# Kernel optimization log

Hardware: AMD Instinct MI355X
Metric: run time of the kernel (lower is better)

Reference implementation:

```python
import jax, jax.numpy as jnp
import numpy as np

B, T, C, H = 8, 2048, 1024, 64  # batch, seq_len(block_size), embedding_size, head_size


def setup_inputs() -> dict:
    key = jax.random.key(0)
    kx, kk, kq, kv = jax.random.split(key, 4)
    x = jax.random.normal(kx, (B, T, C), dtype=jnp.float32)
    # nn.Linear(C, H, bias=False) weights, stored as [in, out] for x @ W
    s = 1.0 / np.sqrt(C)
    Wk = jax.random.uniform(kk, (C, H), dtype=jnp.float32, minval=-s, maxval=s)
    Wq = jax.random.uniform(kq, (C, H), dtype=jnp.float32, minval=-s, maxval=s)
    Wv = jax.random.uniform(kv, (C, H), dtype=jnp.float32, minval=-s, maxval=s)
    return {"x": x, "Wk": Wk, "Wq": Wq, "Wv": Wv}


def reference(x, Wk, Wq, Wv):
    Bx, Tx, Cx = x.shape
    k = jnp.einsum('btc,ch->bth', x, Wk)
    q = jnp.einsum('btc,ch->bth', x, Wq)
    v = jnp.einsum('btc,ch->bth', x, Wv)
    # NOTE: original scales by embedding dim C ** -0.5, not head_size
    scores = jnp.einsum('bth,bsh->bts', q, k) * (Cx ** -0.5)  # [B,T,T]
    causal = jnp.tril(jnp.ones((Tx, Tx), dtype=bool))
    scores = jnp.where(causal, scores, -jnp.inf)
    attn = jax.nn.softmax(scores, axis=-1)
    # dropout is identity in eval/deterministic mode
    out = jnp.einsum('bts,bsh->bth', attn, v)  # [B,T,H]
    return out
```

## Files before the change

kernel.cpp:

```cpp
#include <hip/hip_runtime.h>
#include <hip/hip_bf16.h>
#include <math.h>


#define BT 16384
#define TSEQ 2048
#define XST 72

typedef __attribute__((ext_vector_type(8))) __bf16 bf16x8;
typedef __attribute__((ext_vector_type(8))) unsigned short ushort8;
typedef __attribute__((ext_vector_type(4))) float floatx4;

#define MFMA16(a, b, c) __builtin_amdgcn_mfma_f32_16x16x32_bf16( \
    __builtin_bit_cast(bf16x8, (a)), __builtin_bit_cast(bf16x8, (b)), (c), 0, 0, 0)

__device__ inline unsigned short f2bf(float f) {
  unsigned u = __builtin_bit_cast(unsigned, f);
  u += 0x7FFFu + ((u >> 16) & 1u);
  return (unsigned short)(u >> 16);
}
__device__ inline float bf2f(unsigned short s) {
  return __builtin_bit_cast(float, (unsigned)s << 16);
}
__device__ inline unsigned long long pack4bf(floatx4 f) {
  return (unsigned long long)f2bf(f[0]) | ((unsigned long long)f2bf(f[1]) << 16) |
         ((unsigned long long)f2bf(f[2]) << 32) | ((unsigned long long)f2bf(f[3]) << 48);
}

__global__ __launch_bounds__(256) void wt2_kernel(
    const float* __restrict__ Wq, const float* __restrict__ Wk,
    const float* __restrict__ Wv, unsigned short* __restrict__ Wt2) {
  __shared__ float ls[64][65];
  const int m = blockIdx.x >> 4;
  const int kci = blockIdx.x & 15;
  const int c0 = kci << 6;
  const float* __restrict__ W = (m == 0) ? Wq : (m == 1) ? Wk : Wv;
  const int tid = threadIdx.x;
#pragma unroll
  for (int i = 0; i < 16; ++i) {
    int idx = tid + (i << 8);
    int cl = idx >> 6, h = idx & 63;
    ls[cl][h] = W[(c0 + cl) * 64 + h];
  }
  __syncthreads();
  const int w = tid >> 6, lane = tid & 63;
  const int quad = lane >> 4, l16 = lane & 15;
  const int nt = (m << 2) + w;
#pragma unroll
  for (int half = 0; half < 2; ++half) {
    ushort8 t;
#pragma unroll
    for (int j = 0; j < 8; ++j)
      t[j] = f2bf(ls[(half << 5) + (quad << 3) + j][(w << 4) + l16]);
    *(ushort8*)(Wt2 + ((size_t)(((nt << 4) + kci) * 2 + half) << 9) +
                (lane << 3)) = t;
  }
}

__global__ __launch_bounds__(256) void qkv_mfma(
    const float* __restrict__ x, const unsigned short* __restrict__ Wt2,
    unsigned short* __restrict__ Qf, unsigned short* __restrict__ Kf,
    unsigned short* __restrict__ Vf) {
  __shared__ unsigned short region[4][16 * XST];
  __shared__ float red[2][12][64][4];

  const int tid = threadIdx.x;
  const int w = tid >> 6, lane = tid & 63;
  const int quad = lane >> 4, l16 = lane & 15;
  const int r0 = blockIdx.x << 4;
  const float* __restrict__ xw = x + (size_t)r0 * 1024 + (w << 8);
  const int srow = lane >> 4, scol = (lane & 15) << 2;

  floatx4 acc[12];
#pragma unroll
  for (int i = 0; i < 12; ++i) acc[i] = (floatx4){0.f, 0.f, 0.f, 0.f};

  floatx4 pf[2][4];
#pragma unroll
  for (int i = 0; i < 4; ++i)
    pf[0][i] = *(const floatx4*)(xw + (size_t)((i << 2) + srow) * 1024 + scol);
#pragma unroll
  for (int i = 0; i < 4; ++i)
    pf[1][i] = *(const floatx4*)(xw + (size_t)((i << 2) + srow) * 1024 + 64 + scol);

  unsigned short* buf = &region[w][0];
#pragma unroll
  for (int it = 0; it < 4; ++it) {
#pragma unroll
    for (int i = 0; i < 4; ++i)
      *(unsigned long long*)&buf[((i << 2) + srow) * XST + scol] =
          pack4bf(pf[it & 1][i]);
    if (it < 2) {
#pragma unroll
      for (int i = 0; i < 4; ++i)
        pf[it & 1][i] = *(const floatx4*)(xw + (size_t)((i << 2) + srow) * 1024 +
                                          ((it + 2) << 6) + scol);
    }
    ushort8 a0 = *(const ushort8*)&buf[l16 * XST + (quad << 3)];
    ushort8 a1 = *(const ushort8*)&buf[l16 * XST + 32 + (quad << 3)];
    const int kci = (w << 2) + it;
    const unsigned short* bbase = Wt2 + ((size_t)kci << 10) + ((size_t)lane << 3);
#pragma unroll
    for (int nt = 0; nt < 12; ++nt) {
      const unsigned short* bp = bbase + ((size_t)nt << 14);
      ushort8 b0 = *(const ushort8*)bp;
      ushort8 b1 = *(const ushort8*)(bp + 512);
      acc[nt] = MFMA16(a0, b0, acc[nt]);
      acc[nt] = MFMA16(a1, b1, acc[nt]);
    }
  }

  if (w == 1) {
#pragma unroll
    for (int nt = 0; nt < 12; ++nt) *(floatx4*)&red[0][nt][lane][0] = acc[nt];
  } else if (w == 3) {
#pragma unroll
    for (int nt = 0; nt < 12; ++nt) *(floatx4*)&red[1][nt][lane][0] = acc[nt];
  }
  __syncthreads();
  if (w == 0) {
#pragma unroll
    for (int nt = 0; nt < 12; ++nt) acc[nt] += *(const floatx4*)&red[0][nt][lane][0];
  } else if (w == 2) {
#pragma unroll
    for (int nt = 0; nt < 12; ++nt) acc[nt] += *(const floatx4*)&red[1][nt][lane][0];
  }
  __syncthreads();
  if (w == 2) {
#pragma unroll
    for (int nt = 0; nt < 12; ++nt) *(floatx4*)&red[0][nt][lane][0] = acc[nt];
  }
  __syncthreads();
  unsigned short* qs = &region[0][0];
  unsigned short* ks = qs + 16 * XST;
  unsigned short* vt = ks + 16 * XST;
  if (w == 0) {
#pragma unroll
    for (int nt = 0; nt < 12; ++nt) acc[nt] += *(const floatx4*)&red[0][nt][lane][0];
#pragma unroll
    for (int nt = 0; nt < 4; ++nt)
#pragma unroll
      for (int r = 0; r < 4; ++r)
        qs[((quad << 2) + r) * XST + (nt << 4) + l16] = f2bf(acc[nt][r]);
#pragma unroll
    for (int nt = 4; nt < 8; ++nt)
#pragma unroll
      for (int r = 0; r < 4; ++r)
        ks[((quad << 2) + r) * XST + ((nt - 4) << 4) + l16] = f2bf(acc[nt][r]);
#pragma unroll
    for (int nt = 8; nt < 12; ++nt)
#pragma unroll
      for (int r = 0; r < 4; ++r)
        vt[(((nt - 8) << 4) + l16) * 24 + (quad << 2) + r] = f2bf(acc[nt][r]);
  }
  __syncthreads();

  const int b = r0 >> 11;
  const int r16 = (r0 & 2047) >> 4;
  const int st = (r0 & 2047) >> 6;
  const int ntK = (r0 >> 4) & 3;
  const int khV = (r0 >> 5) & 1;
  const int q0v = (r0 >> 3) & 3;
  if (w == 0) {
#pragma unroll
    for (int kh = 0; kh < 2; ++kh) {
      ushort8 t = *(const ushort8*)&qs[l16 * XST + (kh << 5) + (quad << 3)];
      *(ushort8*)(Qf + ((((size_t)b * 128 + r16) * 2 + kh) << 9) + (lane << 3)) = t;
    }
  } else if (w == 1) {
#pragma unroll
    for (int kh = 0; kh < 2; ++kh) {
      ushort8 t = *(const ushort8*)&ks[l16 * XST + (kh << 5) + (quad << 3)];
      *(ushort8*)(Kf + ((((size_t)(b * 32 + st) * 4 + ntK) * 2 + kh) << 9) +
                  (lane << 3)) = t;
    }
  } else {
    if ((quad >> 1) == (q0v >> 1)) {
#pragma unroll
      for (int sub = 0; sub < 2; ++sub) {
        const int ntE = ((w - 2) << 1) + sub;
        ushort8 t = *(const ushort8*)&vt[((ntE << 4) + l16) * 24 +
                                         ((quad - q0v) << 3)];
        *(ushort8*)(Vf + ((((size_t)(b * 32 + st) * 4 + ntE) * 2 + khV) << 9) +
                    (lane << 3)) = t;
      }
    }
  }
}

__global__ __launch_bounds__(128) void attn_part(
    const unsigned short* __restrict__ Qf, const unsigned short* __restrict__ Kf,
    const unsigned short* __restrict__ Vf, float* __restrict__ part) {
  __shared__ unsigned short Pw[2][16 * XST];

  const int tid = threadIdx.x;
  const int w = tid >> 6, lane = tid & 63;
  const int quad = lane >> 4, l16 = lane & 15;
  const int b = blockIdx.x / 288;
  const int rem = blockIdx.x - b * 288;
  const int e = rem >> 1, half = rem & 1;
  int g = 0;
#pragma unroll
  for (int gg = 1; gg < 8; ++gg) g += (e >= 2 * gg * (gg + 1)) ? 1 : 0;
  const int rem2 = e - 2 * g * (g + 1);
  const int qt = (g << 2) + rem2 / (g + 1);
  const int ch = rem2 - (rem2 / (g + 1)) * (g + 1);
  const int s0 = ch << 2;
  const int s1 = min(s0 + 4, qt + 1);
  const int rg = (half << 1) + w;
  const int r16 = (qt << 2) + rg;

  const unsigned short* qbase =
      Qf + ((((size_t)b * 128 + r16) * 2) << 9) + (lane << 3);
  ushort8 qf0 = *(const ushort8*)qbase;
  ushort8 qf1 = *(const ushort8*)(qbase + 512);

  floatx4 acc[4], lacc;
#pragma unroll
  for (int nt = 0; nt < 4; ++nt) acc[nt] = (floatx4){0.f, 0.f, 0.f, 0.f};
  lacc = (floatx4){0.f, 0.f, 0.f, 0.f};
  const ushort8 ones = {0x3F80, 0x3F80, 0x3F80, 0x3F80,
                        0x3F80, 0x3F80, 0x3F80, 0x3F80};

#define KVIDX(ss, nt, kh) \
  (((((size_t)(b * 32 + (ss)) << 2) + (nt)) * 2 + (kh)) << 9)

  ushort8 bk[4][2];
#pragma unroll
  for (int nt = 0; nt < 4; ++nt)
#pragma unroll
    for (int kh = 0; kh < 2; ++kh)
      bk[nt][kh] = *(const ushort8*)(Kf + KVIDX(s0, nt, kh) + (lane << 3));

  for (int s = s0; s < s1; ++s) {
    const int sn = (s + 1 < s1) ? s + 1 : s;
    ushort8 bv[4][2];
#pragma unroll
    for (int nt = 0; nt < 4; ++nt)
#pragma unroll
      for (int kh = 0; kh < 2; ++kh)
        bv[nt][kh] = *(const ushort8*)(Vf + KVIDX(s, nt, kh) + (lane << 3));
    ushort8 bkn[4][2];
#pragma unroll
    for (int nt = 0; nt < 4; ++nt)
#pragma unroll
      for (int kh = 0; kh < 2; ++kh)
        bkn[nt][kh] = *(const ushort8*)(Kf + KVIDX(sn, nt, kh) + (lane << 3));

    floatx4 sf[4];
#pragma unroll
    for (int nt = 0; nt < 4; ++nt) {
      sf[nt] = (floatx4){0.f, 0.f, 0.f, 0.f};
      sf[nt] = MFMA16(qf0, bk[nt][0], sf[nt]);
      sf[nt] = MFMA16(qf1, bk[nt][1], sf[nt]);
    }

    const bool diag = (s == qt);
    const int qrow = (rg << 4) + (quad << 2);
#pragma unroll
    for (int nt = 0; nt < 4; ++nt) {
      const int keyl = (nt << 4) + l16;
#pragma unroll
      for (int r = 0; r < 4; ++r) {
        float ev = __expf(sf[nt][r] * 0.03125f);
        if (diag && keyl > ((qt << 6) - (qt << 6)) + qrow + r) ev = 0.f;
        Pw[w][((quad << 2) + r) * XST + keyl] = f2bf(ev);
      }
    }

#pragma unroll
    for (int kh = 0; kh < 2; ++kh) {
      ushort8 pa = *(const ushort8*)&Pw[w][l16 * XST + (kh << 5) + (quad << 3)];
      lacc = MFMA16(pa, ones, lacc);
#pragma unroll
      for (int nt = 0; nt < 4; ++nt) acc[nt] = MFMA16(pa, bv[nt][kh], acc[nt]);
    }
#pragma unroll
    for (int nt = 0; nt < 4; ++nt) {
      bk[nt][0] = bkn[nt][0];
      bk[nt][1] = bkn[nt][1];
    }
  }
#undef KVIDX

  float* slot = part + (size_t)(b * 144 + e) * 2112;
  if (l16 == 0) {
#pragma unroll
    for (int r = 0; r < 4; ++r) slot[(rg << 4) + (quad << 2) + r] = lacc[r];
  }
  unsigned short* op = (unsigned short*)(slot + 64);
#pragma unroll
  for (int nt = 0; nt < 4; ++nt)
#pragma unroll
    for (int r = 0; r < 4; ++r)
      op[((rg << 4) + (quad << 2) + r) * 64 + (nt << 4) + l16] = f2bf(acc[nt][r]);
}

__global__ __launch_bounds__(256) void attn_combine(
    const float* __restrict__ part, float* __restrict__ out) {
  const int rh = blockIdx.x & 1;
  const int bqt = blockIdx.x >> 1;
  const int b = bqt >> 5, qt = bqt & 31;
  const int tid = threadIdx.x;
  const int row = (rh << 5) + (tid >> 3);
  const int hseg = (tid & 7) << 3;
  const int g = qt >> 2;
  const int nch = g + 1;
  const int ebase = 2 * g * (g + 1) + (qt & 3) * (g + 1);

  float l = 0.f;
  float ov[8];
#pragma unroll
  for (int i = 0; i < 8; ++i) ov[i] = 0.f;
  for (int c = 0; c < nch; ++c) {
    const float* slot = part + (size_t)(b * 144 + ebase + c) * 2112;
    l += slot[row];
    ushort8 o0 = *(const ushort8*)((const unsigned short*)(slot + 64) +
                                   row * 64 + hseg);
#pragma unroll
    for (int i = 0; i < 8; ++i) ov[i] += bf2f(o0[i]);
  }
  const float inv = 1.f / l;
  float* o = out + ((size_t)(b * TSEQ + (qt << 6) + row)) * 64 + hseg;
#pragma unroll
  for (int i = 0; i < 8; ++i) o[i] = ov[i] * inv;
}

extern "C" void kernel_launch(void* const* d_in, const int* in_sizes, int n_in,
                              void* d_out, int out_size, void* d_ws, size_t ws_size,
                              hipStream_t stream) {
  const float* x  = (const float*)d_in[0];
  const float* Wk = (const float*)d_in[1];
  const float* Wq = (const float*)d_in[2];
  const float* Wv = (const float*)d_in[3];

  unsigned short* Qfw = (unsigned short*)d_ws;
  unsigned short* Kfw = Qfw + (size_t)BT * 64;
  unsigned short* Vfw = Kfw + (size_t)BT * 64;
  unsigned short* Wt2 = Vfw + (size_t)BT * 64;
  float* part = (float*)(Wt2 + 3 * 64 * 1024);

  wt2_kernel<<<48, 256, 0, stream>>>(Wq, Wk, Wv, Wt2);
  qkv_mfma<<<1024, 256, 0, stream>>>(x, Wt2, Qfw, Kfw, Vfw);
  attn_part<<<2304, 128, 0, stream>>>(Qfw, Kfw, Vfw, part);
  attn_combine<<<512, 256, 0, stream>>>(part, (float*)d_out);
}
```

Before: 142.7 us.

## Fuse attention combine into partial kernel via atomic last-block reduction

Removes the separate attn_combine launch. Each attention block now covers all four 16-row groups of a query tile with 256 threads, and an atomic per-tile counter lets the last-finishing chunk block do the reduction. Tiles with a single chunk write the output directly, skipping the partial buffer. The QKV projection loads x straight into MFMA operand registers instead of staging it through LDS, and the softmax exponent uses exp2f with a pre-scaled constant. The cost is threadfence plus atomic synchronisation, and a counter that has to be zeroed on every call by wt2_kernel.

```diff
diff --git a/kernel.cpp b/kernel.cpp
--- a/kernel.cpp
+++ b/kernel.cpp
@@ -22,14 +22,18 @@
 __device__ inline float bf2f(unsigned short s) {
   return __builtin_bit_cast(float, (unsigned)s << 16);
 }
-__device__ inline unsigned long long pack4bf(floatx4 f) {
-  return (unsigned long long)f2bf(f[0]) | ((unsigned long long)f2bf(f[1]) << 16) |
-         ((unsigned long long)f2bf(f[2]) << 32) | ((unsigned long long)f2bf(f[3]) << 48);
+__device__ inline ushort8 pack8(floatx4 a, floatx4 b) {
+  ushort8 t;
+  t[0] = f2bf(a[0]); t[1] = f2bf(a[1]); t[2] = f2bf(a[2]); t[3] = f2bf(a[3]);
+  t[4] = f2bf(b[0]); t[5] = f2bf(b[1]); t[6] = f2bf(b[2]); t[7] = f2bf(b[3]);
+  return t;
 }
 
 __global__ __launch_bounds__(256) void wt2_kernel(
     const float* __restrict__ Wq, const float* __restrict__ Wk,
-    const float* __restrict__ Wv, unsigned short* __restrict__ Wt2) {
+    const float* __restrict__ Wv, unsigned short* __restrict__ Wt2,
+    int* __restrict__ cnt) {
+  if (blockIdx.x == 0) cnt[threadIdx.x] = 0;
   __shared__ float ls[64][65];
   const int m = blockIdx.x >> 4;
   const int kci = blockIdx.x & 15;
@@ -61,45 +65,29 @@
     const float* __restrict__ x, const unsigned short* __restrict__ Wt2,
     unsigned short* __restrict__ Qf, unsigned short* __restrict__ Kf,
     unsigned short* __restrict__ Vf) {
-  __shared__ unsigned short region[4][16 * XST];
   __shared__ float red[2][12][64][4];
 
   const int tid = threadIdx.x;
   const int w = tid >> 6, lane = tid & 63;
   const int quad = lane >> 4, l16 = lane & 15;
   const int r0 = blockIdx.x << 4;
-  const float* __restrict__ xw = x + (size_t)r0 * 1024 + (w << 8);
-  const int srow = lane >> 4, scol = (lane & 15) << 2;
+  const float* __restrict__ xr =
+      x + (size_t)(r0 + l16) * 1024 + (w << 8) + (quad << 3);
 
   floatx4 acc[12];
 #pragma unroll
   for (int i = 0; i < 12; ++i) acc[i] = (floatx4){0.f, 0.f, 0.f, 0.f};
 
-  floatx4 pf[2][4];
-#pragma unroll
-  for (int i = 0; i < 4; ++i)
-    pf[0][i] = *(const floatx4*)(xw + (size_t)((i << 2) + srow) * 1024 + scol);
-#pragma unroll
-  for (int i = 0; i < 4; ++i)
-    pf[1][i] = *(const floatx4*)(xw + (size_t)((i << 2) + srow) * 1024 + 64 + scol);
-
-  unsigned short* buf = &region[w][0];
 #pragma unroll
   for (int it = 0; it < 4; ++it) {
-#pragma unroll
-    for (int i = 0; i < 4; ++i)
-      *(unsigned long long*)&buf[((i << 2) + srow) * XST + scol] =
-          pack4bf(pf[it & 1][i]);
-    if (it < 2) {
-#pragma unroll
-      for (int i = 0; i < 4; ++i)
-        pf[it & 1][i] = *(const floatx4*)(xw + (size_t)((i << 2) + srow) * 1024 +
-                                          ((it + 2) << 6) + scol);
-    }
-    ushort8 a0 = *(const ushort8*)&buf[l16 * XST + (quad << 3)];
-    ushort8 a1 = *(const ushort8*)&buf[l16 * XST + 32 + (quad << 3)];
-    const int kci = (w << 2) + it;
-    const unsigned short* bbase = Wt2 + ((size_t)kci << 10) + ((size_t)lane << 3);
+    floatx4 f0 = *(const floatx4*)(xr + (it << 6));
+    floatx4 f1 = *(const floatx4*)(xr + (it << 6) + 4);
+    floatx4 f2 = *(const floatx4*)(xr + (it << 6) + 32);
+    floatx4 f3 = *(const floatx4*)(xr + (it << 6) + 36);
+    ushort8 a0 = pack8(f0, f1);
+    ushort8 a1 = pack8(f2, f3);
+    const unsigned short* bbase =
+        Wt2 + ((size_t)((w << 2) + it) << 10) + ((size_t)lane << 3);
 #pragma unroll
     for (int nt = 0; nt < 12; ++nt) {
       const unsigned short* bp = bbase + ((size_t)nt << 14);
@@ -131,9 +119,10 @@
     for (int nt = 0; nt < 12; ++nt) *(floatx4*)&red[0][nt][lane][0] = acc[nt];
   }
   __syncthreads();
-  unsigned short* qs = &region[0][0];
-  unsigned short* ks = qs + 16 * XST;
-  unsigned short* vt = ks + 16 * XST;
+  unsigned short* su = (unsigned short*)&red[1][0][0][0];
+  unsigned short* qs = su;
+  unsigned short* ks = su + 16 * XST;
+  unsigned short* vt = su + 32 * XST;
   if (w == 0) {
 #pragma unroll
     for (int nt = 0; nt < 12; ++nt) acc[nt] += *(const floatx4*)&red[0][nt][lane][0];
@@ -188,27 +177,27 @@
   }
 }
 
-__global__ __launch_bounds__(128) void attn_part(
+__global__ __launch_bounds__(256) void attn_part(
     const unsigned short* __restrict__ Qf, const unsigned short* __restrict__ Kf,
-    const unsigned short* __restrict__ Vf, float* __restrict__ part) {
-  __shared__ unsigned short Pw[2][16 * XST];
+    const unsigned short* __restrict__ Vf, float* __restrict__ part,
+    int* __restrict__ cnt, float* __restrict__ out) {
+  __shared__ unsigned short Pw[4][16 * XST];
+  __shared__ int flag;
 
   const int tid = threadIdx.x;
   const int w = tid >> 6, lane = tid & 63;
   const int quad = lane >> 4, l16 = lane & 15;
-  const int b = blockIdx.x / 288;
-  const int rem = blockIdx.x - b * 288;
-  const int e = rem >> 1, half = rem & 1;
+  const int b = blockIdx.x / 144;
+  const int e = blockIdx.x - b * 144;
   int g = 0;
 #pragma unroll
   for (int gg = 1; gg < 8; ++gg) g += (e >= 2 * gg * (gg + 1)) ? 1 : 0;
-  const int rem2 = e - 2 * g * (g + 1);
-  const int qt = (g << 2) + rem2 / (g + 1);
-  const int ch = rem2 - (rem2 / (g + 1)) * (g + 1);
+  const int rem = e - 2 * g * (g + 1);
+  const int qt = (g << 2) + rem / (g + 1);
+  const int ch = rem - (rem / (g + 1)) * (g + 1);
   const int s0 = ch << 2;
   const int s1 = min(s0 + 4, qt + 1);
-  const int rg = (half << 1) + w;
-  const int r16 = (qt << 2) + rg;
+  const int r16 = (qt << 2) + w;
 
   const unsigned short* qbase =
       Qf + ((((size_t)b * 128 + r16) * 2) << 9) + (lane << 3);
@@ -256,14 +245,14 @@
     }
 
     const bool diag = (s == qt);
-    const int qrow = (rg << 4) + (quad << 2);
+    const int qrow = (w << 4) + (quad << 2);
 #pragma unroll
     for (int nt = 0; nt < 4; ++nt) {
       const int keyl = (nt << 4) + l16;
 #pragma unroll
       for (int r = 0; r < 4; ++r) {
-        float ev = __expf(sf[nt][r] * 0.03125f);
-        if (diag && keyl > ((qt << 6) - (qt << 6)) + qrow + r) ev = 0.f;
+        float ev = exp2f(sf[nt][r] * 0.04508422f);
+        if (diag && keyl > qrow + r) ev = 0.f;
         Pw[w][((quad << 2) + r) * XST + keyl] = f2bf(ev);
       }
     }
@@ -283,47 +272,62 @@
   }
 #undef KVIDX
 
+  const int nch = g + 1;
+  if (nch == 1) {
+#pragma unroll
+    for (int r = 0; r < 4; ++r) {
+      const float inv = 1.f / lacc[r];
+      const size_t orow =
+          (size_t)b * TSEQ + (qt << 6) + (w << 4) + (quad << 2) + r;
+#pragma unroll
+      for (int nt = 0; nt < 4; ++nt)
+        out[orow * 64 + (nt << 4) + l16] = acc[nt][r] * inv;
+    }
+    return;
+  }
+
   float* slot = part + (size_t)(b * 144 + e) * 2112;
   if (l16 == 0) {
 #pragma unroll
-    for (int r = 0; r < 4; ++r) slot[(rg << 4) + (quad << 2) + r] = lacc[r];
+    for (int r = 0; r < 4; ++r) slot[(w << 4) + (quad << 2) + r] = lacc[r];
   }
   unsigned short* op = (unsigned short*)(slot + 64);
 #pragma unroll
   for (int nt = 0; nt < 4; ++nt)
 #pragma unroll
     for (int r = 0; r < 4; ++r)
-      op[((rg << 4) + (quad << 2) + r) * 64 + (nt << 4) + l16] = f2bf(acc[nt][r]);
-}
-
-__global__ __launch_bounds__(256) void attn_combine(
-    const float* __restrict__ part, float* __restrict__ out) {
-  const int rh = blockIdx.x & 1;
-  const int bqt = blockIdx.x >> 1;
-  const int b = bqt >> 5, qt = bqt & 31;
-  const int tid = threadIdx.x;
-  const int row = (rh << 5) + (tid >> 3);
-  const int hseg = (tid & 7) << 3;
-  const int g = qt >> 2;
-  const int nch = g + 1;
-  const int ebase = 2 * g * (g + 1) + (qt & 3) * (g + 1);
-
+      op[((w << 4) + (quad << 2) + r) * 64 + (nt << 4) + l16] = f2bf(acc[nt][r]);
+
+  __syncthreads();
+  if (tid == 0) {
+    __threadfence();
+    flag = (atomicAdd(&cnt[(b << 5) + qt], 1) == nch - 1) ? 1 : 0;
+  }
+  __syncthreads();
+  if (!flag) return;
+
+  __threadfence();
+  const int row = tid >> 2, hseg = (tid & 3) << 4;
+  const int ebase = e - ch;
   float l = 0.f;
-  float ov[8];
-#pragma unroll
-  for (int i = 0; i < 8; ++i) ov[i] = 0.f;
+  float ov[16];
+#pragma unroll
+  for (int i = 0; i < 16; ++i) ov[i] = 0.f;
   for (int c = 0; c < nch; ++c) {
-    const float* slot = part + (size_t)(b * 144 + ebase + c) * 2112;
-    l += slot[row];
-    ushort8 o0 = *(const ushort8*)((const unsigned short*)(slot + 64) +
-                                   row * 64 + hseg);
+    const float* sl = part + (size_t)(b * 144 + ebase + c) * 2112;
+    l += sl[row];
+    const unsigned short* o16 = (const unsigned short*)(sl + 64) + row * 64 + hseg;
+    ushort8 o0 = *(const ushort8*)o16;
+    ushort8 o1 = *(const ushort8*)(o16 + 8);
 #pragma unroll
     for (int i = 0; i < 8; ++i) ov[i] += bf2f(o0[i]);
+#pragma unroll
+    for (int i = 0; i < 8; ++i) ov[8 + i] += bf2f(o1[i]);
   }
   const float inv = 1.f / l;
-  float* o = out + ((size_t)(b * TSEQ + (qt << 6) + row)) * 64 + hseg;
-#pragma unroll
-  for (int i = 0; i < 8; ++i) o[i] = ov[i] * inv;
+  float* o = out + ((size_t)b * TSEQ + (qt << 6) + row) * 64 + hseg;
+#pragma unroll
+  for (int i = 0; i < 16; ++i) o[i] = ov[i] * inv;
 }
 
 extern "C" void kernel_launch(void* const* d_in, const int* in_sizes, int n_in,
@@ -339,9 +343,9 @@
   unsigned short* Vfw = Kfw + (size_t)BT * 64;
   unsigned short* Wt2 = Vfw + (size_t)BT * 64;
   float* part = (float*)(Wt2 + 3 * 64 * 1024);
-
-  wt2_kernel<<<48, 256, 0, stream>>>(Wq, Wk, Wv, Wt2);
+  int* cnt = (int*)(part + (size_t)1152 * 2112);
+
+  wt2_kernel<<<48, 256, 0, stream>>>(Wq, Wk, Wv, Wt2, cnt);
   qkv_mfma<<<1024, 256, 0, stream>>>(x, Wt2, Qfw, Kfw, Vfw);
-  attn_part<<<2304, 128, 0, stream>>>(Qfw, Kfw, Vfw, part);
-  attn_combine<<<512, 256, 0, stream>>>(part, (float*)d_out);
-}
+  attn_part<<<1152, 256, 0, stream>>>(Qfw, Kfw, Vfw, part, cnt, (float*)d_out);
+}
```

New measurement: 254.7 us. +78.5%, slower.

## Process two 16-row query tiles per wave to reuse K/V loads

Applied to the files above, without the earlier changes.

Each wave of attn_part now handles 32 query rows (two 16-row MFMA tiles) instead of 16, so every K and V fragment loaded from global memory feeds twice as many MFMAs, and the grid is halved. The software prefetch of the next K block is dropped in favour of loading K and V together each iteration, and exp is rewritten as exp2f with a prescaled constant. The cost is more registers per wave, fewer blocks in flight, and no longer overlapping the next K load with compute.

```diff
diff --git a/kernel.cpp b/kernel.cpp
--- a/kernel.cpp
+++ b/kernel.cpp
@@ -191,94 +191,92 @@
 __global__ __launch_bounds__(128) void attn_part(
     const unsigned short* __restrict__ Qf, const unsigned short* __restrict__ Kf,
     const unsigned short* __restrict__ Vf, float* __restrict__ part) {
-  __shared__ unsigned short Pw[2][16 * XST];
+  __shared__ unsigned short Pw[2][32 * XST];
 
   const int tid = threadIdx.x;
   const int w = tid >> 6, lane = tid & 63;
   const int quad = lane >> 4, l16 = lane & 15;
-  const int b = blockIdx.x / 288;
-  const int rem = blockIdx.x - b * 288;
-  const int e = rem >> 1, half = rem & 1;
+  const int b = blockIdx.x / 144;
+  const int e = blockIdx.x - b * 144;
   int g = 0;
 #pragma unroll
   for (int gg = 1; gg < 8; ++gg) g += (e >= 2 * gg * (gg + 1)) ? 1 : 0;
-  const int rem2 = e - 2 * g * (g + 1);
-  const int qt = (g << 2) + rem2 / (g + 1);
-  const int ch = rem2 - (rem2 / (g + 1)) * (g + 1);
+  const int rem = e - 2 * g * (g + 1);
+  const int qt = (g << 2) + rem / (g + 1);
+  const int ch = rem - (rem / (g + 1)) * (g + 1);
   const int s0 = ch << 2;
   const int s1 = min(s0 + 4, qt + 1);
-  const int rg = (half << 1) + w;
-  const int r16 = (qt << 2) + rg;
-
-  const unsigned short* qbase =
-      Qf + ((((size_t)b * 128 + r16) * 2) << 9) + (lane << 3);
-  ushort8 qf0 = *(const ushort8*)qbase;
-  ushort8 qf1 = *(const ushort8*)(qbase + 512);
-
-  floatx4 acc[4], lacc;
-#pragma unroll
-  for (int nt = 0; nt < 4; ++nt) acc[nt] = (floatx4){0.f, 0.f, 0.f, 0.f};
-  lacc = (floatx4){0.f, 0.f, 0.f, 0.f};
+
+  ushort8 qf[2][2];
+#pragma unroll
+  for (int mh = 0; mh < 2; ++mh) {
+    const unsigned short* qbase =
+        Qf + ((((size_t)b * 128 + (qt << 2) + (w << 1) + mh) * 2) << 9) +
+        (lane << 3);
+    qf[mh][0] = *(const ushort8*)qbase;
+    qf[mh][1] = *(const ushort8*)(qbase + 512);
+  }
+
+  floatx4 acc[2][4], lacc[2];
+#pragma unroll
+  for (int mh = 0; mh < 2; ++mh) {
+#pragma unroll
+    for (int nt = 0; nt < 4; ++nt) acc[mh][nt] = (floatx4){0.f, 0.f, 0.f, 0.f};
+    lacc[mh] = (floatx4){0.f, 0.f, 0.f, 0.f};
+  }
   const ushort8 ones = {0x3F80, 0x3F80, 0x3F80, 0x3F80,
                         0x3F80, 0x3F80, 0x3F80, 0x3F80};
 
 #define KVIDX(ss, nt, kh) \
   (((((size_t)(b * 32 + (ss)) << 2) + (nt)) * 2 + (kh)) << 9)
 
-  ushort8 bk[4][2];
-#pragma unroll
-  for (int nt = 0; nt < 4; ++nt)
-#pragma unroll
-    for (int kh = 0; kh < 2; ++kh)
-      bk[nt][kh] = *(const ushort8*)(Kf + KVIDX(s0, nt, kh) + (lane << 3));
-
   for (int s = s0; s < s1; ++s) {
-    const int sn = (s + 1 < s1) ? s + 1 : s;
-    ushort8 bv[4][2];
+    ushort8 bk[4][2], bv[4][2];
 #pragma unroll
     for (int nt = 0; nt < 4; ++nt)
 #pragma unroll
-      for (int kh = 0; kh < 2; ++kh)
+      for (int kh = 0; kh < 2; ++kh) {
+        bk[nt][kh] = *(const ushort8*)(Kf + KVIDX(s, nt, kh) + (lane << 3));
         bv[nt][kh] = *(const ushort8*)(Vf + KVIDX(s, nt, kh) + (lane << 3));
-    ushort8 bkn[4][2];
-#pragma unroll
-    for (int nt = 0; nt < 4; ++nt)
-#pragma unroll
-      for (int kh = 0; kh < 2; ++kh)
-        bkn[nt][kh] = *(const ushort8*)(Kf + KVIDX(sn, nt, kh) + (lane << 3));
-
-    floatx4 sf[4];
-#pragma unroll
-    for (int nt = 0; nt < 4; ++nt) {
-      sf[nt] = (floatx4){0.f, 0.f, 0.f, 0.f};
-      sf[nt] = MFMA16(qf0, bk[nt][0], sf[nt]);
-      sf[nt] = MFMA16(qf1, bk[nt][1], sf[nt]);
-    }
+      }
+
+    floatx4 sf[2][4];
+#pragma unroll
+    for (int mh = 0; mh < 2; ++mh)
+#pragma unroll
+      for (int nt = 0; nt < 4; ++nt) {
+        sf[mh][nt] = (floatx4){0.f, 0.f, 0.f, 0.f};
+        sf[mh][nt] = MFMA16(qf[mh][0], bk[nt][0], sf[mh][nt]);
+        sf[mh][nt] = MFMA16(qf[mh][1], bk[nt][1], sf[mh][nt]);
+      }
 
     const bool diag = (s == qt);
-    const int qrow = (rg << 4) + (quad << 2);
-#pragma unroll
-    for (int nt = 0; nt < 4; ++nt) {
-      const int keyl = (nt << 4) + l16;
-#pragma unroll
-      for (int r = 0; r < 4; ++r) {
-        float ev = __expf(sf[nt][r] * 0.03125f);
-        if (diag && keyl > ((qt << 6) - (qt << 6)) + qrow + r) ev = 0.f;
-        Pw[w][((quad << 2) + r) * XST + keyl] = f2bf(ev);
+#pragma unroll
+    for (int mh = 0; mh < 2; ++mh) {
+      const int qrow = (w << 5) + (mh << 4) + (quad << 2);
+#pragma unroll
+      for (int nt = 0; nt < 4; ++nt) {
+        const int keyl = (nt << 4) + l16;
+#pragma unroll
+        for (int r = 0; r < 4; ++r) {
+          float ev = exp2f(sf[mh][nt][r] * 0.04508422f);
+          if (diag && keyl > qrow + r) ev = 0.f;
+          Pw[w][((mh << 4) + (quad << 2) + r) * XST + keyl] = f2bf(ev);
+        }
       }
     }
 
 #pragma unroll
     for (int kh = 0; kh < 2; ++kh) {
-      ushort8 pa = *(const ushort8*)&Pw[w][l16 * XST + (kh << 5) + (quad << 3)];
-      lacc = MFMA16(pa, ones, lacc);
-#pragma unroll
-      for (int nt = 0; nt < 4; ++nt) acc[nt] = MFMA16(pa, bv[nt][kh], acc[nt]);
-    }
-#pragma unroll
-    for (int nt = 0; nt < 4; ++nt) {
-      bk[nt][0] = bkn[nt][0];
-      bk[nt][1] = bkn[nt][1];
+#pragma unroll
+      for (int mh = 0; mh < 2; ++mh) {
+        ushort8 pa = *(const ushort8*)&Pw[w][((mh << 4) + l16) * XST +
+                                             (kh << 5) + (quad << 3)];
+        lacc[mh] = MFMA16(pa, ones, lacc[mh]);
+#pragma unroll
+        for (int nt = 0; nt < 4; ++nt)
+          acc[mh][nt] = MFMA16(pa, bv[nt][kh], acc[mh][nt]);
+      }
     }
   }
 #undef KVIDX
@@ -286,14 +284,20 @@
   float* slot = part + (size_t)(b * 144 + e) * 2112;
   if (l16 == 0) {
 #pragma unroll
-    for (int r = 0; r < 4; ++r) slot[(rg << 4) + (quad << 2) + r] = lacc[r];
+    for (int mh = 0; mh < 2; ++mh)
+#pragma unroll
+      for (int r = 0; r < 4; ++r)
+        slot[(w << 5) + (mh << 4) + (quad << 2) + r] = lacc[mh][r];
   }
   unsigned short* op = (unsigned short*)(slot + 64);
 #pragma unroll
-  for (int nt = 0; nt < 4; ++nt)
-#pragma unroll
-    for (int r = 0; r < 4; ++r)
-      op[((rg << 4) + (quad << 2) + r) * 64 + (nt << 4) + l16] = f2bf(acc[nt][r]);
+  for (int mh = 0; mh < 2; ++mh)
+#pragma unroll
+    for (int nt = 0; nt < 4; ++nt)
+#pragma unroll
+      for (int r = 0; r < 4; ++r)
+        op[((w << 5) + (mh << 4) + (quad << 2) + r) * 64 + (nt << 4) + l16] =
+            f2bf(acc[mh][nt][r]);
 }
 
 __global__ __launch_bounds__(256) void attn_combine(
@@ -342,6 +346,6 @@
 
   wt2_kernel<<<48, 256, 0, stream>>>(Wq, Wk, Wv, Wt2);
   qkv_mfma<<<1024, 256, 0, stream>>>(x, Wt2, Qfw, Kfw, Vfw);
-  attn_part<<<2304, 128, 0, stream>>>(Qfw, Kfw, Vfw, part);
+  attn_part<<<1152, 128, 0, stream>>>(Qfw, Kfw, Vfw, part);
   attn_combine<<<512, 256, 0, stream>>>(part, (float*)d_out);
 }
```

New measurement: 145.9 us. 1.02x slower.
